# Kernel optimization log

Measured on AMD Instinct MI355X. Metric: run time of the kernel, lower is better.

Reference implementation:

```python
import jax, jax.numpy as jnp
import numpy as np

C_S, C_Z, C_ATOM, H, RBF = 128, 64, 16, 4, 16
N_RES, E_RES, N_ATOM, E_ATOM = 1000, 4000, 14000, 784000


def _p(key, shape, scale=0.05):
    return (jax.random.normal(key, shape, dtype=jnp.float32) * scale)


def setup_inputs() -> dict:
    key = jax.random.key(0)
    ks = jax.random.split(key, 24)
    inp = {
        "node_features": jax.random.normal(ks[0], (N_RES, C_S), dtype=jnp.float32),
        "res_edge_features": jax.random.normal(ks[1], (E_RES, C_Z), dtype=jnp.float32),
        "res_edge_index": jax.random.randint(ks[2], (2, E_RES), 0, N_RES),
        "atom_features": jax.random.normal(ks[3], (N_ATOM, C_ATOM), dtype=jnp.float32),
        "atom_coords": jax.random.normal(ks[4], (N_ATOM, 3), dtype=jnp.float32),
        "cross_atom_edge_index": jax.random.randint(ks[5], (2, E_ATOM), 0, N_ATOM),
        "atom_edge_to_res_edge": jax.random.randint(ks[6], (E_ATOM,), 0, E_RES),
        # atom_dist_embed MLP: RBF -> RBF -> RBF -> H
        "rbf_w1": _p(ks[7], (RBF, RBF)), "rbf_b1": jnp.zeros((RBF,), jnp.float32),
        "rbf_w2": _p(ks[8], (RBF, RBF)), "rbf_b2": jnp.zeros((RBF,), jnp.float32),
        "rbf_w3": _p(ks[9], (RBF, H)),  "rbf_b3": jnp.zeros((H,), jnp.float32),
        # res_level_bias MLP: (2*c_s + c_z) -> c_atom -> H
        "rb_w1": _p(ks[10], (2 * C_S + C_Z, C_ATOM)), "rb_b1": jnp.zeros((C_ATOM,), jnp.float32),
        "rb_w2": _p(ks[11], (C_ATOM, H)), "rb_b2": jnp.zeros((H,), jnp.float32),
        # q / kv / out projections
        "wq": _p(ks[12], (C_ATOM, C_ATOM * H)),     "bq": jnp.zeros((C_ATOM * H,), jnp.float32),
        "wkv": _p(ks[13], (C_ATOM, 2 * C_ATOM * H)), "bkv": jnp.zeros((2 * C_ATOM * H,), jnp.float32),
        "wo": _p(ks[14], (C_ATOM * H, C_ATOM)),     "bo": jnp.zeros((C_ATOM,), jnp.float32),
    }
    return inp


def _rbf(d, d_min=0.0, d_max=20.0, d_count=RBF):
    mu = jnp.linspace(d_min, d_max, d_count, dtype=jnp.float32)
    sigma = (d_max - d_min) / d_count
    return jnp.exp(-(((d[..., None] - mu) / sigma) ** 2))


def _seg_softmax(x, idx, n_seg):
    # scatter-softmax over segments (pyg_utils.softmax), per head column
    m = jax.ops.segment_max(x, idx, num_segments=n_seg)
    e = jnp.exp(x - m[idx])
    s = jax.ops.segment_sum(e, idx, num_segments=n_seg)
    return e / (s[idx] + 1e-16)


def reference(node_features, res_edge_features, res_edge_index, atom_features,
              atom_coords, cross_atom_edge_index, atom_edge_to_res_edge,
              rbf_w1, rbf_b1, rbf_w2, rbf_b2, rbf_w3, rbf_b3,
              rb_w1, rb_b1, rb_w2, rb_b2, wq, bq, wkv, bkv, wo, bo,
              eps=1e-8):
    src = cross_atom_edge_index[1]
    dst = cross_atom_edge_index[0]

    # RBF distance bias  [E_atom, H]
    vec = atom_coords[dst] - atom_coords[src]
    d = jnp.linalg.norm(vec + eps, axis=-1)
    h = jax.nn.relu(_rbf(d) @ rbf_w1 + rbf_b1)
    h = jax.nn.relu(h @ rbf_w2 + rbf_b2)
    atom_dist_bias = h @ rbf_w3 + rbf_b3

    # residue-level bias  [E_res, H]
    cat = jnp.concatenate([res_edge_features,
                           node_features[res_edge_index[0]],
                           node_features[res_edge_index[1]]], axis=-1)
    res_level_bias = jax.nn.relu(cat @ rb_w1 + rb_b1) @ rb_w2 + rb_b2

    # gathered q / k / v  [E_atom, H, c_atom]
    q = (atom_features @ wq + bq)[src].reshape(-1, H, C_ATOM)
    kv = (atom_features @ wkv + bkv)[dst].reshape(-1, H, 2 * C_ATOM)
    k, v = kv[..., :C_ATOM], kv[..., C_ATOM:]

    R = jnp.einsum('ehc,ehc->eh', q, k) / np.sqrt(C_ATOM)
    R = R + res_level_bias[atom_edge_to_res_edge] + atom_dist_bias

    # atom-level scatter-softmax over edges grouped by src atom
    alpha = _seg_softmax(R, src, N_ATOM)

    # residue-level: scatter-mean of scores per residue edge, then softmax by dst res
    cnt = jax.ops.segment_sum(jnp.ones((R.shape[0],), R.dtype),
                              atom_edge_to_res_edge, num_segments=E_RES)
    block_r = jax.ops.segment_sum(R, atom_edge_to_res_edge, num_segments=E_RES)
    block_r = block_r / jnp.clip(cnt, 1.0)[:, None]
    beta = _seg_softmax(block_r, res_edge_index[1], N_RES)

    w = alpha * beta[atom_edge_to_res_edge]           # [E_atom, H]
    atom_update = jax.ops.segment_sum(w[..., None] * v, src, num_segments=N_ATOM)
    return atom_update.reshape(-1, H * C_ATOM) @ wo + bo
```

## Files before the change

kernel.cpp:

```cpp
#include <hip/hip_runtime.h>

#define NH 4
#define N_RES 1000
#define E_RES 4000
#define N_ATOM 14000
#define E_ATOM 784000
#define MAXS 128
#define NBRE 256
#define TABN 16385
#define TINV 512.0f

#define BUILD_BLKS ((E_ATOM + 255) / 256)
#define PROJ_BLKS ((N_ATOM * 192 + 255) / 256)
#define RLB_BLKS (E_RES / 4)
#define TAB_BLKS ((TABN + 255) / 256)

typedef float f32x4 __attribute__((ext_vector_type(4)));

__device__ __forceinline__ unsigned enc_f(float f) {
  unsigned u = __float_as_uint(f);
  return (u & 0x80000000u) ? ~u : (u | 0x80000000u);
}
__device__ __forceinline__ float dec_f(unsigned e) {
  unsigned u = (e & 0x80000000u) ? (e & 0x7FFFFFFFu) : ~e;
  return __uint_as_float(u);
}

__global__ __launch_bounds__(256) void kA(
    const int* __restrict__ cei, const int* __restrict__ aer,
    int* __restrict__ cnt_src, unsigned* __restrict__ pay,
    const float* __restrict__ af, const float* __restrict__ wq,
    const float* __restrict__ bq, const float* __restrict__ wkv,
    const float* __restrict__ bkv, float* __restrict__ Qa,
    float* __restrict__ Ka, float* __restrict__ Va,
    const float* __restrict__ ref_, const float* __restrict__ nf,
    const int* __restrict__ rei, const float* __restrict__ w1,
    const float* __restrict__ b1, const float* __restrict__ w2,
    const float* __restrict__ b2, float* __restrict__ rlb,
    const float* __restrict__ rw1, const float* __restrict__ rb1,
    const float* __restrict__ rw2, const float* __restrict__ rb2,
    const float* __restrict__ rw3, const float* __restrict__ rb3,
    f32x4* __restrict__ tab) {
  int b = blockIdx.x;
  if (b < BUILD_BLKS) {
    int e = b * 256 + threadIdx.x;
    if (e < E_ATOM) {
      int src = cei[E_ATOM + e];
      int dst = cei[e];
      int re = aer[e];
      int slot = atomicAdd(&cnt_src[src], 1);
      if (slot >= MAXS) slot = MAXS - 1;
      pay[(size_t)src * MAXS + slot] = (unsigned)dst | ((unsigned)re << 16);
    }
  } else if (b < BUILD_BLKS + PROJ_BLKS) {
    int tid = (b - BUILD_BLKS) * 256 + threadIdx.x;
    if (tid < N_ATOM * 192) {
      int a = tid / 192, j = tid % 192;
      const float* row = af + a * 16;
      if (j < 64) {
        float acc = bq[j];
#pragma unroll
        for (int i = 0; i < 16; ++i) acc += row[i] * wq[i * 64 + j];
        Qa[a * 64 + j] = acc;
      } else if (j < 128) {
        int jj = j - 64;
        int col = ((jj >> 4) << 5) + (jj & 15);
        float acc = bkv[col];
#pragma unroll
        for (int i = 0; i < 16; ++i) acc += row[i] * wkv[i * 128 + col];
        Ka[a * 64 + jj] = acc;
      } else {
        int jj = j - 128;
        int col = ((jj >> 4) << 5) + 16 + (jj & 15);
        float acc = bkv[col];
#pragma unroll
        for (int i = 0; i < 16; ++i) acc += row[i] * wkv[i * 128 + col];
        Va[a * 64 + jj] = acc;
      }
    }
  } else if (b < BUILD_BLKS + PROJ_BLKS + RLB_BLKS) {
    __shared__ float hid[4][16];
    int sub = threadIdx.x >> 6, l = threadIdx.x & 63;
    int r = (b - BUILD_BLKS - PROJ_BLKS) * 4 + sub;
    int r0 = rei[r], r1 = rei[E_RES + r];
    int j = l >> 2, pq = l & 3;
    float acc = 0.f;
    for (int i = pq; i < 320; i += 4) {
      float cc;
      if (i < 64) cc = ref_[r * 64 + i];
      else if (i < 192) cc = nf[r0 * 128 + (i - 64)];
      else cc = nf[r1 * 128 + (i - 192)];
      acc += cc * w1[i * 16 + j];
    }
    acc += __shfl_xor(acc, 1);
    acc += __shfl_xor(acc, 2);
    if (pq == 0) hid[sub][j] = fmaxf(acc + b1[j], 0.f);
    __syncthreads();
    if (l < 4) {
      float o = b2[l];
#pragma unroll
      for (int jj = 0; jj < 16; ++jj) o += hid[sub][jj] * w2[jj * 4 + l];
      rlb[r * 4 + l] = o;
    }
  } else {
    int i = (b - BUILD_BLKS - PROJ_BLKS - RLB_BLKS) * 256 + threadIdx.x;
    if (i < TABN) {
      float d = (float)i * (1.0f / TINV);
      float rb[16], h1[16], h2[16];
      const float step = 20.0f / 15.0f;
      const float inv_sigma = 1.0f / 1.25f;
#pragma unroll
      for (int jj = 0; jj < 16; ++jj) {
        float t = (d - jj * step) * inv_sigma;
        rb[jj] = __expf(-t * t);
      }
#pragma unroll
      for (int k = 0; k < 16; ++k) {
        float acc = rb1[k];
#pragma unroll
        for (int jj = 0; jj < 16; ++jj) acc += rb[jj] * rw1[jj * 16 + k];
        h1[k] = fmaxf(acc, 0.f);
      }
#pragma unroll
      for (int k = 0; k < 16; ++k) {
        float acc = rb2[k];
#pragma unroll
        for (int jj = 0; jj < 16; ++jj) acc += h1[jj] * rw2[jj * 16 + k];
        h2[k] = fmaxf(acc, 0.f);
      }
      f32x4 o;
#pragma unroll
      for (int h = 0; h < NH; ++h) {
        float acc = rb3[h];
#pragma unroll
        for (int jj = 0; jj < 16; ++jj) acc += h2[jj] * rw3[jj * 4 + h];
        o[h] = acc;
      }
      tab[i] = o;
    }
  }
}

__global__ __launch_bounds__(256) void k_edgeR(
    const int* __restrict__ cnt_src, const unsigned* __restrict__ pay,
    const float* __restrict__ coords, const float* __restrict__ Qa,
    const float* __restrict__ Ka, const float* __restrict__ rlb,
    const f32x4* __restrict__ tab, float* __restrict__ R_slab,
    f32x4* __restrict__ msm, f32x4* __restrict__ mss) {
  int l = threadIdx.x & 63;
  int a = blockIdx.x * 4 + (threadIdx.x >> 6);
  int n = cnt_src[a];
  if (n > MAXS) n = MAXS;
  size_t base = (size_t)a * MAXS;
  float ax = coords[a * 3 + 0], ay = coords[a * 3 + 1], az = coords[a * 3 + 2];
  const float4* qp = (const float4*)(Qa + (size_t)a * 64);
  bool a0 = l < n, a1 = l + 64 < n;
  f32x4 R0, R1;
#pragma unroll
  for (int sl = 0; sl < 2; ++sl) {
    bool act = sl ? a1 : a0;
    f32x4 Rv = {-3.0e38f, -3.0e38f, -3.0e38f, -3.0e38f};
    if (act) {
      int s = l + sl * 64;
      unsigned pr = pay[base + s];
      int dst = (int)(pr & 0xFFFFu);
      int re = (int)(pr >> 16);
      float vx = coords[dst * 3 + 0] - ax + 1e-8f;
      float vy = coords[dst * 3 + 1] - ay + 1e-8f;
      float vz = coords[dst * 3 + 2] - az + 1e-8f;
      float d = sqrtf(vx * vx + vy * vy + vz * vz);
      float x = d * TINV;
      int i = (int)x;
      if (i > TABN - 2) i = TABN - 2;
      float fr = x - (float)i;
      f32x4 t0 = tab[i], t1 = tab[i + 1];
      f32x4 adb = t0 + (t1 - t0) * fr;
      const float4* kp = (const float4*)(Ka + (size_t)dst * 64);
      float4 rlb4 = *(const float4*)(rlb + re * 4);
      const float* rlbp = (const float*)&rlb4;
#pragma unroll
      for (int h = 0; h < NH; ++h) {
        float dot = 0.f;
#pragma unroll
        for (int v4 = 0; v4 < 4; ++v4) {
          float4 q4 = qp[h * 4 + v4];
          float4 k4 = kp[h * 4 + v4];
          dot += q4.x * k4.x + q4.y * k4.y + q4.z * k4.z + q4.w * k4.w;
        }
        Rv[h] = dot * 0.25f + rlbp[h] + adb[h];
      }
      __builtin_nontemporal_store(Rv, (f32x4*)(R_slab + (base + s) * 4));
    }
    if (sl) R1 = Rv; else R0 = Rv;
  }
  f32x4 mx;
#pragma unroll
  for (int h = 0; h < NH; ++h) mx[h] = fmaxf(R0[h], R1[h]);
#pragma unroll
  for (int off = 1; off < 64; off <<= 1) {
#pragma unroll
    for (int h = 0; h < NH; ++h) mx[h] = fmaxf(mx[h], __shfl_xor(mx[h], off));
  }
  f32x4 ex;
#pragma unroll
  for (int h = 0; h < NH; ++h)
    ex[h] = (a0 ? __expf(R0[h] - mx[h]) : 0.f) +
            (a1 ? __expf(R1[h] - mx[h]) : 0.f);
#pragma unroll
  for (int off = 1; off < 64; off <<= 1) {
#pragma unroll
    for (int h = 0; h < NH; ++h) ex[h] += __shfl_xor(ex[h], off);
  }
  if (l == 0) {
    msm[a] = mx;
    mss[a] = ex;
  }
}

__global__ __launch_bounds__(1024) void k_re2(
    const int* __restrict__ cnt_src, const unsigned* __restrict__ pay,
    const float* __restrict__ R_slab, int* __restrict__ cntg,
    float* __restrict__ br_g) {
  __shared__ __align__(16) unsigned char smraw[64000];
  int* scnt = (int*)smraw;
  float* sbr = (float*)smraw;
  int tid = threadIdx.x;
  int bid = blockIdx.x;
  int wv = tid >> 6, lane = tid & 63;
  int gw = bid * 16 + wv;
  for (int j = tid; j < E_RES; j += 1024) scnt[j] = 0;
  __syncthreads();
  for (int a = gw; a < N_ATOM; a += NBRE * 16) {
    int n = cnt_src[a];
    if (n > MAXS) n = MAXS;
    size_t base = (size_t)a * MAXS;
    for (int i = lane; i < n; i += 64) {
      int re = (int)(pay[base + i] >> 16);
      atomicAdd(&scnt[re], 1);
    }
  }
  __syncthreads();
  for (int j = tid; j < E_RES; j += 1024) cntg[bid * E_RES + j] = scnt[j];
  __syncthreads();
  for (int j = tid; j < E_RES * 4; j += 1024) sbr[j] = 0.f;
  __syncthreads();
  for (int a = gw; a < N_ATOM; a += NBRE * 16) {
    int n = cnt_src[a];
    if (n > MAXS) n = MAXS;
    size_t base = (size_t)a * MAXS;
    for (int i = lane; i < n; i += 64) {
      int re = (int)(pay[base + i] >> 16);
      f32x4 r = *(const f32x4*)(R_slab + (base + i) * 4);
      atomicAdd(&sbr[re * 4 + 0], r[0]);
      atomicAdd(&sbr[re * 4 + 1], r[1]);
      atomicAdd(&sbr[re * 4 + 2], r[2]);
      atomicAdd(&sbr[re * 4 + 3], r[3]);
    }
  }
  __syncthreads();
  for (int j = tid; j < E_RES * 4; j += 1024)
    br_g[(size_t)bid * E_RES * 4 + j] = sbr[j];
}

__global__ __launch_bounds__(256) void k_red(const float* __restrict__ br_g,
                                             const int* __restrict__ cntg,
                                             float* __restrict__ block_r) {
  int t = blockIdx.x * blockDim.x + threadIdx.x;
  if (t >= E_RES * 4) return;
  int r = t >> 2;
  float s = 0.f;
  int c = 0;
  for (int b = 0; b < NBRE; ++b) {
    s += br_g[(size_t)b * E_RES * 4 + t];
    c += cntg[b * E_RES + r];
  }
  block_r[t] = s / fmaxf((float)c, 1.0f);
}

__global__ __launch_bounds__(1024) void k_br23(
    const float* __restrict__ block_r, const int* __restrict__ rei,
    float* __restrict__ beta) {
  __shared__ unsigned resm[N_RES * 4];
  __shared__ float ress[N_RES * 4];
  int tid = threadIdx.x;
  for (int j = tid; j < N_RES * 4; j += 1024) { resm[j] = 0u; ress[j] = 0.f; }
  __syncthreads();
  float brv[4][4];
  int r1v[4];
  for (int k = 0; k < 4; ++k) {
    int r = tid + k * 1024;
    if (r < E_RES) {
      r1v[k] = rei[E_RES + r];
#pragma unroll
      for (int h = 0; h < 4; ++h) {
        brv[k][h] = block_r[r * 4 + h];
        atomicMax(&resm[r1v[k] * 4 + h], enc_f(brv[k][h]));
      }
    }
  }
  __syncthreads();
  for (int k = 0; k < 4; ++k) {
    int r = tid + k * 1024;
    if (r < E_RES) {
#pragma unroll
      for (int h = 0; h < 4; ++h)
        atomicAdd(&ress[r1v[k] * 4 + h],
                  __expf(brv[k][h] - dec_f(resm[r1v[k] * 4 + h])));
    }
  }
  __syncthreads();
  for (int k = 0; k < 4; ++k) {
    int r = tid + k * 1024;
    if (r < E_RES) {
#pragma unroll
      for (int h = 0; h < 4; ++h)
        beta[r * 4 + h] = __expf(brv[k][h] - dec_f(resm[r1v[k] * 4 + h])) /
                          (ress[r1v[k] * 4 + h] + 1e-16f);
    }
  }
}

__global__ __launch_bounds__(256) void k_src(
    const int* __restrict__ cnt_src, const unsigned* __restrict__ pay,
    const float* __restrict__ R_slab, const float* __restrict__ beta,
    const float* __restrict__ Va, const f32x4* __restrict__ msm,
    const f32x4* __restrict__ mss, const float* __restrict__ wo,
    const float* __restrict__ bo, float* __restrict__ out) {
  __shared__ float sau[4][64];
  int wv = threadIdx.x >> 6, l = threadIdx.x & 63;
  int wid = blockIdx.x * 4 + wv;
  int n = cnt_src[wid];
  if (n > MAXS) n = MAXS;
  int h = l >> 4;
  size_t rbase = (size_t)wid * MAXS;
  f32x4 m4 = msm[wid], s4 = mss[wid];
  float mh = m4[h];
  float sden = s4[h] + 1e-16f;
  float acc = 0.f;
#pragma unroll 2
  for (int i = 0; i < n; ++i) {
    unsigned pr = pay[rbase + i];
    int dst = (int)(pr & 0xFFFFu);
    int re = (int)(pr >> 16);
    float rv = R_slab[(rbase + i) * 4 + h];
    float bt = beta[re * 4 + h];
    float v = Va[(size_t)dst * 64 + l];
    acc += __expf(rv - mh) * bt * v;
  }
  sau[wv][l] = acc / sden;
  __syncthreads();
  int p = l >> 4, c = l & 15;
  float part = 0.f;
#pragma unroll
  for (int jj = 0; jj < 16; ++jj)
    part += sau[wv][p * 16 + jj] * wo[(p * 16 + jj) * 16 + c];
  part += __shfl_down(part, 32);
  part += __shfl_down(part, 16);
  if (l < 16) out[wid * 16 + c] = part + bo[c];
}

extern "C" void kernel_launch(void* const* d_in, const int* in_sizes, int n_in,
                              void* d_out, int out_size, void* d_ws,
                              size_t ws_size, hipStream_t stream) {
  const float* nf   = (const float*)d_in[0];
  const float* ref_ = (const float*)d_in[1];
  const int*   rei  = (const int*)d_in[2];
  const float* af   = (const float*)d_in[3];
  const float* co   = (const float*)d_in[4];
  const int*   cei  = (const int*)d_in[5];
  const int*   aer  = (const int*)d_in[6];
  const float* rw1  = (const float*)d_in[7];
  const float* rb1  = (const float*)d_in[8];
  const float* rw2  = (const float*)d_in[9];
  const float* rb2  = (const float*)d_in[10];
  const float* rw3  = (const float*)d_in[11];
  const float* rb3  = (const float*)d_in[12];
  const float* w1   = (const float*)d_in[13];
  const float* b1   = (const float*)d_in[14];
  const float* w2   = (const float*)d_in[15];
  const float* b2   = (const float*)d_in[16];
  const float* wq   = (const float*)d_in[17];
  const float* bq   = (const float*)d_in[18];
  const float* wkv  = (const float*)d_in[19];
  const float* bkv  = (const float*)d_in[20];
  const float* wo   = (const float*)d_in[21];
  const float* bo   = (const float*)d_in[22];
  float* out = (float*)d_out;

  float* ws = (float*)d_ws;
  float*    Qa      = ws;
  float*    Ka      = Qa + 896000;
  float*    Va      = Ka + 896000;
  float*    rlb     = Va + 896000;
  float*    R_slab  = rlb + 16000;
  unsigned* pay     = (unsigned*)(R_slab + 7168000);
  float*    br_g    = (float*)(pay + 1792000);
  int*      cntg    = (int*)(br_g + 4096000);
  int*      cnt_src = cntg + 1024000;
  float*    block_r = (float*)(cnt_src + 14000);
  f32x4*    tab     = (f32x4*)(block_r + 16000);
  f32x4*    msm     = (f32x4*)((float*)tab + 65544);
  f32x4*    mss     = (f32x4*)((float*)msm + 56000);
  float*    beta    = Ka + 16000;

  hipMemsetAsync((void*)cnt_src, 0, 14000 * 4, stream);

  kA<<<BUILD_BLKS + PROJ_BLKS + RLB_BLKS + TAB_BLKS, 256, 0, stream>>>(
      cei, aer, cnt_src, pay, af, wq, bq, wkv, bkv, Qa, Ka, Va, ref_, nf, rei,
      w1, b1, w2, b2, rlb, rw1, rb1, rw2, rb2, rw3, rb3, tab);
  k_edgeR<<<N_ATOM / 4, 256, 0, stream>>>(cnt_src, pay, co, Qa, Ka, rlb, tab,
                                          R_slab, msm, mss);
  k_re2<<<NBRE, 1024, 0, stream>>>(cnt_src, pay, R_slab, cntg, br_g);
  k_red<<<(E_RES * 4 + 255) / 256, 256, 0, stream>>>(br_g, cntg, block_r);
  k_br23<<<1, 1024, 0, stream>>>(block_r, rei, beta);
  k_src<<<N_ATOM / 4, 256, 0, stream>>>(cnt_src, pay, R_slab, beta, Va, msm,
                                        mss, wo, bo, out);
}
```

Measured before the change: 252.4 us.

## Replace global-atomic CSR build with block histogram, prefix offsets, and scatter

Measured after the change: 247.6 us. No clear change (-1.9%).

```diff
diff --git a/kernel.cpp b/kernel.cpp
--- a/kernel.cpp
+++ b/kernel.cpp
@@ -9,8 +9,10 @@
 #define NBRE 256
 #define TABN 16385
 #define TINV 512.0f
-
-#define BUILD_BLKS ((E_ATOM + 255) / 256)
+#define NHB 256
+#define EPB 3063
+
+#define HIST_BLKS NHB
 #define PROJ_BLKS ((N_ATOM * 192 + 255) / 256)
 #define RLB_BLKS (E_RES / 4)
 #define TAB_BLKS ((TABN + 255) / 256)
@@ -27,8 +29,7 @@
 }
 
 __global__ __launch_bounds__(256) void kA(
-    const int* __restrict__ cei, const int* __restrict__ aer,
-    int* __restrict__ cnt_src, unsigned* __restrict__ pay,
+    const int* __restrict__ cei, int* __restrict__ ghist,
     const float* __restrict__ af, const float* __restrict__ wq,
     const float* __restrict__ bq, const float* __restrict__ wkv,
     const float* __restrict__ bkv, float* __restrict__ Qa,
@@ -41,19 +42,27 @@
     const float* __restrict__ rw2, const float* __restrict__ rb2,
     const float* __restrict__ rw3, const float* __restrict__ rb3,
     f32x4* __restrict__ tab) {
+  __shared__ unsigned lhist[N_ATOM / 2];
   int b = blockIdx.x;
-  if (b < BUILD_BLKS) {
-    int e = b * 256 + threadIdx.x;
-    if (e < E_ATOM) {
+  if (b < HIST_BLKS) {
+    int t = threadIdx.x;
+    for (int j = t; j < N_ATOM / 2; j += 256) lhist[j] = 0u;
+    __syncthreads();
+    int e0 = b * EPB;
+    int e1 = e0 + EPB;
+    if (e1 > E_ATOM) e1 = E_ATOM;
+    for (int e = e0 + t; e < e1; e += 256) {
       int src = cei[E_ATOM + e];
-      int dst = cei[e];
-      int re = aer[e];
-      int slot = atomicAdd(&cnt_src[src], 1);
-      if (slot >= MAXS) slot = MAXS - 1;
-      pay[(size_t)src * MAXS + slot] = (unsigned)dst | ((unsigned)re << 16);
-    }
-  } else if (b < BUILD_BLKS + PROJ_BLKS) {
-    int tid = (b - BUILD_BLKS) * 256 + threadIdx.x;
+      atomicAdd(&lhist[src >> 1], (src & 1) ? 65536u : 1u);
+    }
+    __syncthreads();
+    int2* gh = (int2*)(ghist + (size_t)b * N_ATOM);
+    for (int j = t; j < N_ATOM / 2; j += 256) {
+      unsigned v = lhist[j];
+      gh[j] = make_int2((int)(v & 0xFFFFu), (int)(v >> 16));
+    }
+  } else if (b < HIST_BLKS + PROJ_BLKS) {
+    int tid = (b - HIST_BLKS) * 256 + threadIdx.x;
     if (tid < N_ATOM * 192) {
       int a = tid / 192, j = tid % 192;
       const float* row = af + a * 16;
@@ -78,10 +87,10 @@
         Va[a * 64 + jj] = acc;
       }
     }
-  } else if (b < BUILD_BLKS + PROJ_BLKS + RLB_BLKS) {
+  } else if (b < HIST_BLKS + PROJ_BLKS + RLB_BLKS) {
     __shared__ float hid[4][16];
     int sub = threadIdx.x >> 6, l = threadIdx.x & 63;
-    int r = (b - BUILD_BLKS - PROJ_BLKS) * 4 + sub;
+    int r = (b - HIST_BLKS - PROJ_BLKS) * 4 + sub;
     int r0 = rei[r], r1 = rei[E_RES + r];
     int j = l >> 2, pq = l & 3;
     float acc = 0.f;
@@ -103,7 +112,7 @@
       rlb[r * 4 + l] = o;
     }
   } else {
-    int i = (b - BUILD_BLKS - PROJ_BLKS - RLB_BLKS) * 256 + threadIdx.x;
+    int i = (b - HIST_BLKS - PROJ_BLKS - RLB_BLKS) * 256 + threadIdx.x;
     if (i < TABN) {
       float d = (float)i * (1.0f / TINV);
       float rb[16], h1[16], h2[16];
@@ -138,6 +147,41 @@
       }
       tab[i] = o;
     }
+  }
+}
+
+__global__ __launch_bounds__(256) void k_ofs(const int* __restrict__ ghist,
+                                             int* __restrict__ ofs,
+                                             int* __restrict__ cnt_src) {
+  int s = blockIdx.x * blockDim.x + threadIdx.x;
+  if (s >= N_ATOM) return;
+  int run = 0;
+  for (int b = 0; b < NHB; ++b) {
+    int v = ghist[(size_t)b * N_ATOM + s];
+    ofs[(size_t)b * N_ATOM + s] = run;
+    run += v;
+  }
+  cnt_src[s] = (run > MAXS) ? MAXS : run;
+}
+
+__global__ __launch_bounds__(256) void k_scat(
+    const int* __restrict__ cei, const int* __restrict__ aer,
+    const int* __restrict__ ofs, unsigned* __restrict__ pay) {
+  __shared__ int lbase[N_ATOM];
+  int b = blockIdx.x, t = threadIdx.x;
+  const int* orow = ofs + (size_t)b * N_ATOM;
+  for (int j = t; j < N_ATOM; j += 256) lbase[j] = orow[j];
+  __syncthreads();
+  int e0 = b * EPB;
+  int e1 = e0 + EPB;
+  if (e1 > E_ATOM) e1 = E_ATOM;
+  for (int e = e0 + t; e < e1; e += 256) {
+    int src = cei[E_ATOM + e];
+    int dst = cei[e];
+    int re = aer[e];
+    int slot = atomicAdd(&lbase[src], 1);
+    if (slot < MAXS)
+      pay[(size_t)src * MAXS + slot] = (unsigned)dst | ((unsigned)re << 16);
   }
 }
 
@@ -401,13 +445,15 @@
   f32x4*    tab     = (f32x4*)(block_r + 16000);
   f32x4*    msm     = (f32x4*)((float*)tab + 65544);
   f32x4*    mss     = (f32x4*)((float*)msm + 56000);
+  int*      ghist   = (int*)br_g;
+  int*      ofs     = (int*)R_slab;
   float*    beta    = Ka + 16000;
 
-  hipMemsetAsync((void*)cnt_src, 0, 14000 * 4, stream);
-
-  kA<<<BUILD_BLKS + PROJ_BLKS + RLB_BLKS + TAB_BLKS, 256, 0, stream>>>(
-      cei, aer, cnt_src, pay, af, wq, bq, wkv, bkv, Qa, Ka, Va, ref_, nf, rei,
-      w1, b1, w2, b2, rlb, rw1, rb1, rw2, rb2, rw3, rb3, tab);
+  kA<<<HIST_BLKS + PROJ_BLKS + RLB_BLKS + TAB_BLKS, 256, 0, stream>>>(
+      cei, ghist, af, wq, bq, wkv, bkv, Qa, Ka, Va, ref_, nf, rei, w1, b1, w2,
+      b2, rlb, rw1, rb1, rw2, rb2, rw3, rb3, tab);
+  k_ofs<<<(N_ATOM + 255) / 256, 256, 0, stream>>>(ghist, ofs, cnt_src);
+  k_scat<<<NHB, 256, 0, stream>>>(cei, aer, ofs, pay);
   k_edgeR<<<N_ATOM / 4, 256, 0, stream>>>(cnt_src, pay, co, Qa, Ka, rlb, tab,
                                           R_slab, msm, mss);
   k_re2<<<NBRE, 1024, 0, stream>>>(cnt_src, pay, R_slab, cntg, br_g);
```
